# Kernel optimization log

Measured on AMD Instinct MI355X. Metric: run time of the kernel, lower is better.

The kernel has to match this reference:

```python
import jax, jax.numpy as jnp
import numpy as np

ALL_NODE_NUM = 12288
FEA_DIM = 32           # dim2 in DGATNet
BATCH_SIZE = 8
WIN_NUM = 4
POOLED_PER_WIN = 192   # ratio=0.5 of 384 nodes per window graph
N_EDGES = 393216       # avg degree 32


def setup_inputs() -> dict:
    key = jax.random.key(0)
    k1, k2, k3, k4, k5 = jax.random.split(key, 5)
    n_perm = BATCH_SIZE * WIN_NUM * POOLED_PER_WIN  # 6144
    fea = jax.random.normal(k1, (n_perm, FEA_DIM), dtype=jnp.float32)
    # perm: unique sorted node indices kept by the pooling stage
    perm = jnp.sort(jax.random.permutation(k2, ALL_NODE_NUM)[:n_perm]).astype(jnp.int32)
    encoder_edge_index = jax.random.randint(k3, (2, N_EDGES), 0, ALL_NODE_NUM, dtype=jnp.int32)
    encoder_edge_attr = jax.random.uniform(k4, (N_EDGES,), dtype=jnp.float32)
    node_atte_coffe = jax.random.uniform(k5, (BATCH_SIZE * POOLED_PER_WIN,), dtype=jnp.float32)
    return {
        "fea": fea,
        "perm": perm,
        "encoder_edge_index": encoder_edge_index,
        "encoder_edge_attr": encoder_edge_attr,
        "node_atte_coffe": node_atte_coffe,
        "all_node_num": ALL_NODE_NUM,
        "batch_size": BATCH_SIZE,
    }


def reference(fea, perm, encoder_edge_index, encoder_edge_attr, node_atte_coffe,
              all_node_num, batch_size):
    """Faithful JAX translation of DiffusioUnpool.forward (DGATNet.unpool)."""
    n_perm, fea_dim = fea.shape
    slide_win_num = n_perm // node_atte_coffe.shape[0]
    node_num = node_atte_coffe.shape[0] // batch_size

    # ones(B,W,1) @ coffe(B,1,node_num) == tile coefficients over windows
    nac = node_atte_coffe.reshape(batch_size, 1, node_num)
    win_nac = jnp.broadcast_to(nac, (batch_size, slide_win_num, node_num)).reshape(-1)

    # scatter pooled features / coefficients back into the full node set
    x_zero = jnp.zeros((all_node_num, fea_dim), dtype=fea.dtype).at[perm].set(fea)
    atte_zero = jnp.zeros((all_node_num,), dtype=fea.dtype).at[perm].set(win_nac)

    # dense adjacency (duplicate edges sum, as in sparse_coo_tensor + to_dense)
    A = jnp.zeros((all_node_num, all_node_num), dtype=fea.dtype)
    A = A.at[encoder_edge_index[0], encoder_edge_index[1]].add(encoder_edge_attr)
    A = A + jnp.eye(all_node_num, dtype=fea.dtype)  # + I self loops

    d = 1.0 / jnp.sqrt(jnp.sum(A, axis=1))  # diag of D = deg^{-1/2}
    # D A D x  ==  d * (A @ (d * x))
    x = d[:, None] * (A @ (d[:, None] * x_zero))
    atte_updata = d * (A @ (d * atte_zero))
    return x, atte_updata
```

## Files before the change

### kernel.cpp

```cpp
#include <hip/hip_runtime.h>

constexpr int ALL_NODES = 12288;
constexpr int FEA       = 32;
constexpr int N_PERM    = 6144;
constexpr int N_EDGES   = 393216;
constexpr int NODE_NUM  = 192;
constexpr int WINxNODE  = 768;

constexpr int RCAP   = 48;
constexpr int NWORDS = ALL_NODES / 32;
constexpr float FIX   = 16777216.0f;
constexpr float UNFIX = 1.0f / 16777216.0f;

constexpr size_t CNT_OFF    = 0;
constexpr size_t ROWBUF_OFF = CNT_OFF + 2 * (size_t)ALL_NODES;
constexpr size_t BMP_OFF    = ROWBUF_OFF + (size_t)ALL_NODES * RCAP * 2;
constexpr size_t RANK_OFF   = BMP_OFF + NWORDS;

__global__ __launch_bounds__(512) void k_init(const int* __restrict__ perm,
                                              uint4* __restrict__ cnt_v,
                                              unsigned int* __restrict__ bmp,
                                              int* __restrict__ rank) {
    int t = threadIdx.x;
    if (blockIdx.x == 0) {
        __shared__ int pops[NWORDS];
        unsigned bits = 0u;
        if (t < NWORDS) {
            int base = t * 32;
            int loI = 0, hiI = N_PERM;
            while (loI < hiI) {
                int mid = (loI + hiI) >> 1;
                if (perm[mid] < base) loI = mid + 1; else hiI = mid;
            }
            for (int k = loI; k < N_PERM; ++k) {
                int p = perm[k];
                if (p >= base + 32) break;
                bits |= 1u << (p - base);
            }
            bmp[t] = bits;
            pops[t] = __popc(bits);
        }
        __syncthreads();
        for (int off = 1; off < NWORDS; off <<= 1) {
            int v = 0;
            if (t < NWORDS && t >= off) v = pops[t - off];
            __syncthreads();
            if (t < NWORDS) pops[t] += v;
            __syncthreads();
        }
        if (t < NWORDS) rank[t] = pops[t] - __popc(bits);
    } else {
        cnt_v[(blockIdx.x - 1) * 512 + t] = make_uint4(0u, 0u, 0u, 0u);
    }
}

__global__ __launch_bounds__(256) void k_bin(const int* __restrict__ ei0,
                                             const int* __restrict__ ei1,
                                             const float* __restrict__ attr,
                                             const unsigned int* __restrict__ bmp,
                                             const int* __restrict__ rank,
                                             unsigned long long* __restrict__ cnt64,
                                             uint2* __restrict__ rowbuf) {
    int p = blockIdx.x * 256 + threadIdx.x;
    int2   r2 = ((const int2*)ei0)[p];
    int2   c2 = ((const int2*)ei1)[p];
    float2 w2 = ((const float2*)attr)[p];
#pragma unroll
    for (int q = 0; q < 2; ++q) {
        int r = q ? r2.y : r2.x;
        int c = q ? c2.y : c2.x;
        float w = q ? w2.y : w2.x;
        unsigned wfix = __float2uint_rn(w * FIX);
        unsigned word = bmp[c >> 5];
        bool live = (word >> (c & 31)) & 1u;
        unsigned long long add = (unsigned long long)wfix
                               | (live ? (1ULL << 40) : 0ULL);
        unsigned long long old = atomicAdd(cnt64 + r, add);
        if (live) {
            unsigned slot = (unsigned)(old >> 40);
            if (slot < RCAP) {
                int kk = rank[c >> 5] + __popc(word & ((1u << (c & 31)) - 1u));
                rowbuf[(size_t)r * RCAP + slot] =
                    make_uint2(((unsigned)kk << 14) | (unsigned)c, __float_as_uint(w));
            }
        }
    }
}

__device__ __forceinline__ float deg_to_d(unsigned long long cv) {
    unsigned dsum = (unsigned)(cv & 0xFFFFFFFFFFULL);
    return rsqrtf(1.0f + (float)dsum * UNFIX);
}

__global__ __launch_bounds__(256) void k_spmv(const uint2* __restrict__ rowbuf,
                                              const unsigned long long* __restrict__ cnt64,
                                              const float* __restrict__ fea,
                                              const float* __restrict__ nac,
                                              const unsigned int* __restrict__ bmp,
                                              const int* __restrict__ rank,
                                              float* __restrict__ out_x,
                                              float* __restrict__ out_a) {
    int t = threadIdx.x;
    int r = blockIdx.x * 8 + (t >> 5);
    int f = t & 31;
    unsigned long long cv = cnt64[r];
    int n = (int)(cv >> 40); if (n > RCAP) n = RCAP;
    float d_r = deg_to_d(cv);
    const uint2* rp = rowbuf + (size_t)r * RCAP;
    float acc = 0.f, accA = 0.f;
    int i = 0;
    for (; i + 8 <= n; i += 8) {
        uint2 e[8];
#pragma unroll
        for (int q = 0; q < 8; ++q) e[q] = rp[i + q];
        float dci[8], yv[8];
#pragma unroll
        for (int q = 0; q < 8; ++q) {
            dci[q] = deg_to_d(cnt64[e[q].x & 16383]);
            yv[q]  = fea[(size_t)(e[q].x >> 14) * FEA + f];
        }
#pragma unroll
        for (int q = 0; q < 8; ++q)
            acc += __uint_as_float(e[q].y) * dci[q] * yv[q];
        if (f == 0) {
#pragma unroll
            for (int q = 0; q < 8; ++q) {
                int kk = e[q].x >> 14;
                accA += __uint_as_float(e[q].y) * dci[q]
                      * nac[(kk / WINxNODE) * NODE_NUM + (kk % NODE_NUM)];
            }
        }
    }
    for (; i < n; ++i) {
        uint2 e = rp[i];
        int kk = e.x >> 14, c = e.x & 16383;
        float d = deg_to_d(cnt64[c]);
        float w = __uint_as_float(e.y);
        acc += w * d * fea[(size_t)kk * FEA + f];
        if (f == 0)
            accA += w * d * nac[(kk / WINxNODE) * NODE_NUM + (kk % NODE_NUM)];
    }
    unsigned word = bmp[r >> 5];
    float self = 0.f, selfa = 0.f;
    if ((word >> (r & 31)) & 1u) {
        int kkr = rank[r >> 5] + __popc(word & ((1u << (r & 31)) - 1u));
        self  = d_r * fea[(size_t)kkr * FEA + f];
        selfa = d_r * nac[(kkr / WINxNODE) * NODE_NUM + (kkr % NODE_NUM)];
    }
    out_x[(size_t)r * FEA + f] = d_r * (acc + self);
    if (f == 0)
        out_a[r] = d_r * (accA + selfa);
}

extern "C" void kernel_launch(void* const* d_in, const int* in_sizes, int n_in,
                              void* d_out, int out_size, void* d_ws, size_t ws_size,
                              hipStream_t stream) {
    const float* fea  = (const float*)d_in[0];
    const int*   perm = (const int*)d_in[1];
    const int*   ei   = (const int*)d_in[2];
    const float* attr = (const float*)d_in[3];
    const float* nac  = (const float*)d_in[4];

    unsigned int*       ws     = (unsigned int*)d_ws;
    unsigned long long* cnt64  = (unsigned long long*)(ws + CNT_OFF);
    uint2*              rowbuf = (uint2*)(ws + ROWBUF_OFF);
    unsigned int*       bmp    = ws + BMP_OFF;
    int*                rank   = (int*)(ws + RANK_OFF);

    float* out_x = (float*)d_out;
    float* out_a = out_x + ALL_NODES * FEA;

    k_init<<<13,            512, 0, stream>>>(perm, (uint4*)cnt64, bmp, rank);
    k_bin <<<N_EDGES / 512, 256, 0, stream>>>(ei, ei + N_EDGES, attr, bmp, rank,
                                              cnt64, rowbuf);
    k_spmv<<<ALL_NODES / 8, 256, 0, stream>>>(rowbuf, cnt64, fea, nac, bmp, rank,
                                              out_x, out_a);
}
```

Measured before the change: 105.3 us.

## Replicate per-row atomic counters into four copies and precompute degree table

Edge binning now spreads each row's atomic counter and row buffer across four replicas selected by wavefront within the block, which should reduce atomic contention on hot rows. A new kernel sums the replicas into a float degree-normalisation table and packs per-replica edge counts. The SpMV then reads dtab instead of recomputing rsqrt from 64-bit counters, and gathers edges from the four replica segments. This costs an extra launch, a larger workspace to zero, and more index arithmetic in the gather loop. Each replica segment can hold only 24 live edges, so a row whose edges land unevenly across replicas can silently drop entries.

```diff
diff --git a/kernel.cpp b/kernel.cpp
--- a/kernel.cpp
+++ b/kernel.cpp
@@ -7,15 +7,18 @@
 constexpr int NODE_NUM  = 192;
 constexpr int WINxNODE  = 768;
 
-constexpr int RCAP   = 48;
+constexpr int NREP   = 4;
+constexpr int RCAPR  = 24;
 constexpr int NWORDS = ALL_NODES / 32;
 constexpr float FIX   = 16777216.0f;
 constexpr float UNFIX = 1.0f / 16777216.0f;
 
 constexpr size_t CNT_OFF    = 0;
-constexpr size_t ROWBUF_OFF = CNT_OFF + 2 * (size_t)ALL_NODES;
-constexpr size_t BMP_OFF    = ROWBUF_OFF + (size_t)ALL_NODES * RCAP * 2;
+constexpr size_t ROWBUF_OFF = CNT_OFF + 2 * (size_t)NREP * ALL_NODES;
+constexpr size_t BMP_OFF    = ROWBUF_OFF + (size_t)NREP * ALL_NODES * RCAPR * 2;
 constexpr size_t RANK_OFF   = BMP_OFF + NWORDS;
+constexpr size_t DTAB_OFF   = RANK_OFF + NWORDS;
+constexpr size_t NW_OFF     = DTAB_OFF + ALL_NODES;
 
 __global__ __launch_bounds__(512) void k_init(const int* __restrict__ perm,
                                               uint4* __restrict__ cnt_v,
@@ -61,7 +64,9 @@
                                              const int* __restrict__ rank,
                                              unsigned long long* __restrict__ cnt64,
                                              uint2* __restrict__ rowbuf) {
-    int p = blockIdx.x * 256 + threadIdx.x;
+    int t = threadIdx.x;
+    int p = blockIdx.x * 256 + t;
+    int rep = t >> 6;
     int2   r2 = ((const int2*)ei0)[p];
     int2   c2 = ((const int2*)ei1)[p];
     float2 w2 = ((const float2*)attr)[p];
@@ -75,25 +80,39 @@
         bool live = (word >> (c & 31)) & 1u;
         unsigned long long add = (unsigned long long)wfix
                                | (live ? (1ULL << 40) : 0ULL);
-        unsigned long long old = atomicAdd(cnt64 + r, add);
+        size_t rr = (size_t)rep * ALL_NODES + r;
+        unsigned long long old = atomicAdd(cnt64 + rr, add);
         if (live) {
             unsigned slot = (unsigned)(old >> 40);
-            if (slot < RCAP) {
+            if (slot < RCAPR) {
                 int kk = rank[c >> 5] + __popc(word & ((1u << (c & 31)) - 1u));
-                rowbuf[(size_t)r * RCAP + slot] =
+                rowbuf[rr * RCAPR + slot] =
                     make_uint2(((unsigned)kk << 14) | (unsigned)c, __float_as_uint(w));
             }
         }
     }
 }
 
-__device__ __forceinline__ float deg_to_d(unsigned long long cv) {
-    unsigned dsum = (unsigned)(cv & 0xFFFFFFFFFFULL);
-    return rsqrtf(1.0f + (float)dsum * UNFIX);
+__global__ __launch_bounds__(256) void k_deg(const unsigned long long* __restrict__ cnt64,
+                                             float* __restrict__ dtab,
+                                             unsigned int* __restrict__ nwords) {
+    int r = blockIdx.x * 256 + threadIdx.x;
+    unsigned long long c0 = cnt64[r];
+    unsigned long long c1 = cnt64[ALL_NODES + r];
+    unsigned long long c2 = cnt64[2 * ALL_NODES + r];
+    unsigned long long c3 = cnt64[3 * ALL_NODES + r];
+    unsigned long long s = c0 + c1 + c2 + c3;
+    dtab[r] = rsqrtf(1.0f + (float)(unsigned)s * UNFIX);
+    unsigned n0 = (unsigned)(c0 >> 40); if (n0 > RCAPR) n0 = RCAPR;
+    unsigned n1 = (unsigned)(c1 >> 40); if (n1 > RCAPR) n1 = RCAPR;
+    unsigned n2 = (unsigned)(c2 >> 40); if (n2 > RCAPR) n2 = RCAPR;
+    unsigned n3 = (unsigned)(c3 >> 40); if (n3 > RCAPR) n3 = RCAPR;
+    nwords[r] = n0 | (n1 << 8) | (n2 << 16) | (n3 << 24);
 }
 
 __global__ __launch_bounds__(256) void k_spmv(const uint2* __restrict__ rowbuf,
-                                              const unsigned long long* __restrict__ cnt64,
+                                              const float* __restrict__ dtab,
+                                              const unsigned int* __restrict__ nwords,
                                               const float* __restrict__ fea,
                                               const float* __restrict__ nac,
                                               const unsigned int* __restrict__ bmp,
@@ -103,20 +122,27 @@
     int t = threadIdx.x;
     int r = blockIdx.x * 8 + (t >> 5);
     int f = t & 31;
-    unsigned long long cv = cnt64[r];
-    int n = (int)(cv >> 40); if (n > RCAP) n = RCAP;
-    float d_r = deg_to_d(cv);
-    const uint2* rp = rowbuf + (size_t)r * RCAP;
+    float d_r = dtab[r];
+    unsigned nw = nwords[r];
+    int b1 = nw & 255;
+    int b2 = b1 + ((nw >> 8) & 255);
+    int b3 = b2 + ((nw >> 16) & 255);
+    int n  = b3 + (nw >> 24);
     float acc = 0.f, accA = 0.f;
     int i = 0;
     for (; i + 8 <= n; i += 8) {
         uint2 e[8];
 #pragma unroll
-        for (int q = 0; q < 8; ++q) e[q] = rp[i + q];
+        for (int q = 0; q < 8; ++q) {
+            int gi  = i + q;
+            int rep = (gi >= b1) + (gi >= b2) + (gi >= b3);
+            int base = rep == 0 ? 0 : (rep == 1 ? b1 : (rep == 2 ? b2 : b3));
+            e[q] = rowbuf[((size_t)rep * ALL_NODES + r) * RCAPR + (gi - base)];
+        }
         float dci[8], yv[8];
 #pragma unroll
         for (int q = 0; q < 8; ++q) {
-            dci[q] = deg_to_d(cnt64[e[q].x & 16383]);
+            dci[q] = dtab[e[q].x & 16383];
             yv[q]  = fea[(size_t)(e[q].x >> 14) * FEA + f];
         }
 #pragma unroll
@@ -132,9 +158,11 @@
         }
     }
     for (; i < n; ++i) {
-        uint2 e = rp[i];
+        int rep = (i >= b1) + (i >= b2) + (i >= b3);
+        int base = rep == 0 ? 0 : (rep == 1 ? b1 : (rep == 2 ? b2 : b3));
+        uint2 e = rowbuf[((size_t)rep * ALL_NODES + r) * RCAPR + (i - base)];
         int kk = e.x >> 14, c = e.x & 16383;
-        float d = deg_to_d(cnt64[c]);
+        float d = dtab[c];
         float w = __uint_as_float(e.y);
         acc += w * d * fea[(size_t)kk * FEA + f];
         if (f == 0)
@@ -166,13 +194,16 @@
     uint2*              rowbuf = (uint2*)(ws + ROWBUF_OFF);
     unsigned int*       bmp    = ws + BMP_OFF;
     int*                rank   = (int*)(ws + RANK_OFF);
+    float*              dtab   = (float*)(ws + DTAB_OFF);
+    unsigned int*       nwords = ws + NW_OFF;
 
     float* out_x = (float*)d_out;
     float* out_a = out_x + ALL_NODES * FEA;
 
-    k_init<<<13,            512, 0, stream>>>(perm, (uint4*)cnt64, bmp, rank);
+    k_init<<<49,            512, 0, stream>>>(perm, (uint4*)cnt64, bmp, rank);
     k_bin <<<N_EDGES / 512, 256, 0, stream>>>(ei, ei + N_EDGES, attr, bmp, rank,
                                               cnt64, rowbuf);
-    k_spmv<<<ALL_NODES / 8, 256, 0, stream>>>(rowbuf, cnt64, fea, nac, bmp, rank,
+    k_deg <<<ALL_NODES / 256, 256, 0, stream>>>(cnt64, dtab, nwords);
+    k_spmv<<<ALL_NODES / 8, 256, 0, stream>>>(rowbuf, dtab, nwords, fea, nac, bmp, rank,
                                               out_x, out_a);
 }
```

Measured after the change: 111.5 us. 5.9% more time.

## Privatize degree sums in LDS histograms and precompute normalization table

Applied to the files above, without the earlier changes.

Degree sums are no longer built with 64-bit global atomics on every edge. Each block now accumulates a private 12288-entry LDS histogram, writes it to a partials buffer, and a new reduction kernel sums the partials and stores a precomputed deg^-1/2 table. Global atomics are now used only for live-edge slot counters, which are 32-bit. The SpMV reads the float table instead of recomputing rsqrt from 64-bit counters. In exchange there is an extra kernel launch and a roughly 12.5MB partials write and read, and the 48KB LDS histogram per block limits occupancy.

```diff
diff --git a/kernel.cpp b/kernel.cpp
--- a/kernel.cpp
+++ b/kernel.cpp
@@ -9,13 +9,16 @@
 
 constexpr int RCAP   = 48;
 constexpr int NWORDS = ALL_NODES / 32;
+constexpr int NHB    = 256;
 constexpr float FIX   = 16777216.0f;
 constexpr float UNFIX = 1.0f / 16777216.0f;
 
-constexpr size_t CNT_OFF    = 0;
-constexpr size_t ROWBUF_OFF = CNT_OFF + 2 * (size_t)ALL_NODES;
+constexpr size_t CNT32_OFF  = 0;
+constexpr size_t ROWBUF_OFF = CNT32_OFF + (size_t)ALL_NODES;
 constexpr size_t BMP_OFF    = ROWBUF_OFF + (size_t)ALL_NODES * RCAP * 2;
 constexpr size_t RANK_OFF   = BMP_OFF + NWORDS;
+constexpr size_t DTAB_OFF   = RANK_OFF + NWORDS;
+constexpr size_t PART_OFF   = DTAB_OFF + ALL_NODES;
 
 __global__ __launch_bounds__(512) void k_init(const int* __restrict__ perm,
                                               uint4* __restrict__ cnt_v,
@@ -54,30 +57,33 @@
     }
 }
 
-__global__ __launch_bounds__(256) void k_bin(const int* __restrict__ ei0,
+__global__ __launch_bounds__(512) void k_bin(const int* __restrict__ ei0,
                                              const int* __restrict__ ei1,
                                              const float* __restrict__ attr,
                                              const unsigned int* __restrict__ bmp,
                                              const int* __restrict__ rank,
-                                             unsigned long long* __restrict__ cnt64,
-                                             uint2* __restrict__ rowbuf) {
-    int p = blockIdx.x * 256 + threadIdx.x;
-    int2   r2 = ((const int2*)ei0)[p];
-    int2   c2 = ((const int2*)ei1)[p];
-    float2 w2 = ((const float2*)attr)[p];
-#pragma unroll
-    for (int q = 0; q < 2; ++q) {
-        int r = q ? r2.y : r2.x;
-        int c = q ? c2.y : c2.x;
-        float w = q ? w2.y : w2.x;
+                                             unsigned int* __restrict__ cnt32,
+                                             uint2* __restrict__ rowbuf,
+                                             unsigned int* __restrict__ part) {
+    __shared__ unsigned int hist[ALL_NODES];
+    int t = threadIdx.x;
+    uint4* hv = (uint4*)hist;
+#pragma unroll
+    for (int i = 0; i < 6; ++i) hv[t + i * 512] = make_uint4(0u, 0u, 0u, 0u);
+    __syncthreads();
+
+    int base = blockIdx.x * (N_EDGES / NHB);
+#pragma unroll
+    for (int q = 0; q < 3; ++q) {
+        int p = base + q * 512 + t;
+        int   r = ei0[p];
+        int   c = ei1[p];
+        float w = attr[p];
         unsigned wfix = __float2uint_rn(w * FIX);
+        atomicAdd(&hist[r], wfix);
         unsigned word = bmp[c >> 5];
-        bool live = (word >> (c & 31)) & 1u;
-        unsigned long long add = (unsigned long long)wfix
-                               | (live ? (1ULL << 40) : 0ULL);
-        unsigned long long old = atomicAdd(cnt64 + r, add);
-        if (live) {
-            unsigned slot = (unsigned)(old >> 40);
+        if ((word >> (c & 31)) & 1u) {
+            unsigned slot = atomicAdd(cnt32 + r, 1u);
             if (slot < RCAP) {
                 int kk = rank[c >> 5] + __popc(word & ((1u << (c & 31)) - 1u));
                 rowbuf[(size_t)r * RCAP + slot] =
@@ -85,15 +91,33 @@
             }
         }
     }
-}
-
-__device__ __forceinline__ float deg_to_d(unsigned long long cv) {
-    unsigned dsum = (unsigned)(cv & 0xFFFFFFFFFFULL);
-    return rsqrtf(1.0f + (float)dsum * UNFIX);
+    __syncthreads();
+    uint4* pv = (uint4*)(part + (size_t)blockIdx.x * ALL_NODES);
+#pragma unroll
+    for (int i = 0; i < 6; ++i) pv[t + i * 512] = hv[t + i * 512];
+}
+
+__global__ __launch_bounds__(256) void k_deg(const unsigned int* __restrict__ part,
+                                             float* __restrict__ dtab) {
+    __shared__ unsigned int acc[256];
+    int t  = threadIdx.x;
+    int rl = t & 63, s = t >> 6;
+    int r  = blockIdx.x * 64 + rl;
+    unsigned int sum = 0;
+    const unsigned int* p = part + (size_t)(s * 64) * ALL_NODES + r;
+#pragma unroll 8
+    for (int b = 0; b < 64; ++b) sum += p[(size_t)b * ALL_NODES];
+    acc[t] = sum;
+    __syncthreads();
+    if (t < 64) {
+        unsigned int deg = acc[t] + acc[64 + t] + acc[128 + t] + acc[192 + t];
+        dtab[r] = rsqrtf(1.0f + (float)deg * UNFIX);
+    }
 }
 
 __global__ __launch_bounds__(256) void k_spmv(const uint2* __restrict__ rowbuf,
-                                              const unsigned long long* __restrict__ cnt64,
+                                              const unsigned int* __restrict__ cnt32,
+                                              const float* __restrict__ dtab,
                                               const float* __restrict__ fea,
                                               const float* __restrict__ nac,
                                               const unsigned int* __restrict__ bmp,
@@ -103,9 +127,8 @@
     int t = threadIdx.x;
     int r = blockIdx.x * 8 + (t >> 5);
     int f = t & 31;
-    unsigned long long cv = cnt64[r];
-    int n = (int)(cv >> 40); if (n > RCAP) n = RCAP;
-    float d_r = deg_to_d(cv);
+    int n = (int)cnt32[r]; if (n > RCAP) n = RCAP;
+    float d_r = dtab[r];
     const uint2* rp = rowbuf + (size_t)r * RCAP;
     float acc = 0.f, accA = 0.f;
     int i = 0;
@@ -116,7 +139,7 @@
         float dci[8], yv[8];
 #pragma unroll
         for (int q = 0; q < 8; ++q) {
-            dci[q] = deg_to_d(cnt64[e[q].x & 16383]);
+            dci[q] = dtab[e[q].x & 16383];
             yv[q]  = fea[(size_t)(e[q].x >> 14) * FEA + f];
         }
 #pragma unroll
@@ -134,7 +157,7 @@
     for (; i < n; ++i) {
         uint2 e = rp[i];
         int kk = e.x >> 14, c = e.x & 16383;
-        float d = deg_to_d(cnt64[c]);
+        float d = dtab[c];
         float w = __uint_as_float(e.y);
         acc += w * d * fea[(size_t)kk * FEA + f];
         if (f == 0)
@@ -162,17 +185,20 @@
     const float* nac  = (const float*)d_in[4];
 
     unsigned int*       ws     = (unsigned int*)d_ws;
-    unsigned long long* cnt64  = (unsigned long long*)(ws + CNT_OFF);
+    unsigned int*       cnt32  = ws + CNT32_OFF;
     uint2*              rowbuf = (uint2*)(ws + ROWBUF_OFF);
     unsigned int*       bmp    = ws + BMP_OFF;
     int*                rank   = (int*)(ws + RANK_OFF);
+    float*              dtab   = (float*)(ws + DTAB_OFF);
+    unsigned int*       part   = ws + PART_OFF;
 
     float* out_x = (float*)d_out;
     float* out_a = out_x + ALL_NODES * FEA;
 
-    k_init<<<13,            512, 0, stream>>>(perm, (uint4*)cnt64, bmp, rank);
-    k_bin <<<N_EDGES / 512, 256, 0, stream>>>(ei, ei + N_EDGES, attr, bmp, rank,
-                                              cnt64, rowbuf);
-    k_spmv<<<ALL_NODES / 8, 256, 0, stream>>>(rowbuf, cnt64, fea, nac, bmp, rank,
-                                              out_x, out_a);
-}
+    k_init<<<7,               512, 0, stream>>>(perm, (uint4*)cnt32, bmp, rank);
+    k_bin <<<NHB,             512, 0, stream>>>(ei, ei + N_EDGES, attr, bmp, rank,
+                                                cnt32, rowbuf, part);
+    k_deg <<<ALL_NODES / 64,  256, 0, stream>>>(part, dtab);
+    k_spmv<<<ALL_NODES / 8,   256, 0, stream>>>(rowbuf, cnt32, dtab, fea, nac,
+                                                bmp, rank, out_x, out_a);
+}
```

New measurement: 107.8 us. 2.4% more time.

## Fuse init, binning and SpMV into one cooperative kernel with grid syncs

Applied to the files above, without the earlier changes.

Replaces the three separate launches (init bitmap/rank, edge binning with atomics, per-row SpMV) with a single cooperative persistent kernel that uses grid.sync between phases, with the grid sized from occupancy. This is meant to remove launch overhead and inter-kernel gaps. It falls back to the old three-kernel path if the cooperative launch fails. The trade-offs are grid-wide barrier costs, a fixed grid of at most 512 blocks of 512 threads, and unvectorized edge loads in the binning phase.

```diff
diff --git a/kernel.cpp b/kernel.cpp
--- a/kernel.cpp
+++ b/kernel.cpp
@@ -1,4 +1,7 @@
 #include <hip/hip_runtime.h>
+#include <hip/hip_cooperative_groups.h>
+
+namespace cg = cooperative_groups;
 
 constexpr int ALL_NODES = 12288;
 constexpr int FEA       = 32;
@@ -16,6 +19,133 @@
 constexpr size_t ROWBUF_OFF = CNT_OFF + 2 * (size_t)ALL_NODES;
 constexpr size_t BMP_OFF    = ROWBUF_OFF + (size_t)ALL_NODES * RCAP * 2;
 constexpr size_t RANK_OFF   = BMP_OFF + NWORDS;
+
+__device__ __forceinline__ float deg_to_d(unsigned long long cv) {
+    unsigned dsum = (unsigned)(cv & 0xFFFFFFFFFFULL);
+    return rsqrtf(1.0f + (float)dsum * UNFIX);
+}
+
+__global__ __launch_bounds__(512, 4) void k_fused(
+        const float* __restrict__ fea, const int* __restrict__ perm,
+        const int* __restrict__ ei0, const int* __restrict__ ei1,
+        const float* __restrict__ attr, const float* __restrict__ nac,
+        unsigned long long* __restrict__ cnt64, uint2* __restrict__ rowbuf,
+        unsigned int* __restrict__ bmp, int* __restrict__ rank,
+        float* __restrict__ out_x, float* __restrict__ out_a) {
+    cg::grid_group grid = cg::this_grid();
+    const int t     = threadIdx.x;
+    const int b     = blockIdx.x;
+    const int nb    = gridDim.x;
+    const int gtid  = b * 512 + t;
+    const int gsize = nb * 512;
+
+    if (b == 0) {
+        __shared__ int pops[NWORDS];
+        unsigned bits = 0u;
+        if (t < NWORDS) {
+            int base = t * 32;
+            int loI = 0, hiI = N_PERM;
+            while (loI < hiI) {
+                int mid = (loI + hiI) >> 1;
+                if (perm[mid] < base) loI = mid + 1; else hiI = mid;
+            }
+            for (int k = loI; k < N_PERM; ++k) {
+                int p = perm[k];
+                if (p >= base + 32) break;
+                bits |= 1u << (p - base);
+            }
+            bmp[t] = bits;
+            pops[t] = __popc(bits);
+        }
+        __syncthreads();
+        for (int off = 1; off < NWORDS; off <<= 1) {
+            int v = 0;
+            if (t < NWORDS && t >= off) v = pops[t - off];
+            __syncthreads();
+            if (t < NWORDS) pops[t] += v;
+            __syncthreads();
+        }
+        if (t < NWORDS) rank[t] = pops[t] - __popc(bits);
+    } else {
+        int idx = gtid - 512;
+        if (idx < 2 * ALL_NODES / 4)
+            ((uint4*)cnt64)[idx] = make_uint4(0u, 0u, 0u, 0u);
+    }
+    grid.sync();
+
+    for (int e = gtid; e < N_EDGES; e += gsize) {
+        int   r = ei0[e];
+        int   c = ei1[e];
+        float w = attr[e];
+        unsigned wfix = __float2uint_rn(w * FIX);
+        unsigned word = bmp[c >> 5];
+        bool live = (word >> (c & 31)) & 1u;
+        unsigned long long add = (unsigned long long)wfix
+                               | (live ? (1ULL << 40) : 0ULL);
+        unsigned long long old = atomicAdd(cnt64 + r, add);
+        if (live) {
+            unsigned slot = (unsigned)(old >> 40);
+            if (slot < RCAP) {
+                int kk = rank[c >> 5] + __popc(word & ((1u << (c & 31)) - 1u));
+                rowbuf[(size_t)r * RCAP + slot] =
+                    make_uint2(((unsigned)kk << 14) | (unsigned)c, __float_as_uint(w));
+            }
+        }
+    }
+    grid.sync();
+
+    const int f = t & 31;
+    for (int r0 = b * 16; r0 < ALL_NODES; r0 += nb * 16) {
+        int r = r0 + (t >> 5);
+        unsigned long long cv = cnt64[r];
+        int n = (int)(cv >> 40); if (n > RCAP) n = RCAP;
+        float d_r = deg_to_d(cv);
+        const uint2* rp = rowbuf + (size_t)r * RCAP;
+        float acc = 0.f, accA = 0.f;
+        int i = 0;
+        for (; i + 8 <= n; i += 8) {
+            uint2 e[8];
+#pragma unroll
+            for (int q = 0; q < 8; ++q) e[q] = rp[i + q];
+            float dci[8], yv[8];
+#pragma unroll
+            for (int q = 0; q < 8; ++q) {
+                dci[q] = deg_to_d(cnt64[e[q].x & 16383]);
+                yv[q]  = fea[(size_t)(e[q].x >> 14) * FEA + f];
+            }
+#pragma unroll
+            for (int q = 0; q < 8; ++q)
+                acc += __uint_as_float(e[q].y) * dci[q] * yv[q];
+            if (f == 0) {
+#pragma unroll
+                for (int q = 0; q < 8; ++q) {
+                    int kk = e[q].x >> 14;
+                    accA += __uint_as_float(e[q].y) * dci[q]
+                          * nac[(kk / WINxNODE) * NODE_NUM + (kk % NODE_NUM)];
+                }
+            }
+        }
+        for (; i < n; ++i) {
+            uint2 e = rp[i];
+            int kk = e.x >> 14, c = e.x & 16383;
+            float d = deg_to_d(cnt64[c]);
+            float w = __uint_as_float(e.y);
+            acc += w * d * fea[(size_t)kk * FEA + f];
+            if (f == 0)
+                accA += w * d * nac[(kk / WINxNODE) * NODE_NUM + (kk % NODE_NUM)];
+        }
+        unsigned word = bmp[r >> 5];
+        float self = 0.f, selfa = 0.f;
+        if ((word >> (r & 31)) & 1u) {
+            int kkr = rank[r >> 5] + __popc(word & ((1u << (r & 31)) - 1u));
+            self  = d_r * fea[(size_t)kkr * FEA + f];
+            selfa = d_r * nac[(kkr / WINxNODE) * NODE_NUM + (kkr % NODE_NUM)];
+        }
+        out_x[(size_t)r * FEA + f] = d_r * (acc + self);
+        if (f == 0)
+            out_a[r] = d_r * (accA + selfa);
+    }
+}
 
 __global__ __launch_bounds__(512) void k_init(const int* __restrict__ perm,
                                               uint4* __restrict__ cnt_v,
@@ -85,11 +215,6 @@
             }
         }
     }
-}
-
-__device__ __forceinline__ float deg_to_d(unsigned long long cv) {
-    unsigned dsum = (unsigned)(cv & 0xFFFFFFFFFFULL);
-    return rsqrtf(1.0f + (float)dsum * UNFIX);
 }
 
 __global__ __launch_bounds__(256) void k_spmv(const uint2* __restrict__ rowbuf,
@@ -157,7 +282,8 @@
                               hipStream_t stream) {
     const float* fea  = (const float*)d_in[0];
     const int*   perm = (const int*)d_in[1];
-    const int*   ei   = (const int*)d_in[2];
+    const int*   ei0  = (const int*)d_in[2];
+    const int*   ei1  = ei0 + N_EDGES;
     const float* attr = (const float*)d_in[3];
     const float* nac  = (const float*)d_in[4];
 
@@ -170,9 +296,27 @@
     float* out_x = (float*)d_out;
     float* out_a = out_x + ALL_NODES * FEA;
 
-    k_init<<<13,            512, 0, stream>>>(perm, (uint4*)cnt64, bmp, rank);
-    k_bin <<<N_EDGES / 512, 256, 0, stream>>>(ei, ei + N_EDGES, attr, bmp, rank,
-                                              cnt64, rowbuf);
-    k_spmv<<<ALL_NODES / 8, 256, 0, stream>>>(rowbuf, cnt64, fea, nac, bmp, rank,
-                                              out_x, out_a);
-}
+    static int grid_blocks = 0;
+    if (grid_blocks == 0) {
+        int per_cu = 0;
+        if (hipOccupancyMaxActiveBlocksPerMultiprocessor(&per_cu, k_fused, 512, 0)
+                != hipSuccess || per_cu < 1)
+            per_cu = 1;
+        grid_blocks = per_cu * 256;
+        if (grid_blocks > 512) grid_blocks = 512;
+    }
+
+    void* args[] = {(void*)&fea, (void*)&perm, (void*)&ei0, (void*)&ei1,
+                    (void*)&attr, (void*)&nac, (void*)&cnt64, (void*)&rowbuf,
+                    (void*)&bmp, (void*)&rank, (void*)&out_x, (void*)&out_a};
+    hipError_t err = hipLaunchCooperativeKernel((const void*)k_fused,
+                                                dim3(grid_blocks), dim3(512),
+                                                args, 0, stream);
+    if (err != hipSuccess) {
+        k_init<<<13,            512, 0, stream>>>(perm, (uint4*)cnt64, bmp, rank);
+        k_bin <<<N_EDGES / 512, 256, 0, stream>>>(ei0, ei1, attr, bmp, rank,
+                                                  cnt64, rowbuf);
+        k_spmv<<<ALL_NODES / 8, 256, 0, stream>>>(rowbuf, cnt64, fea, nac, bmp,
+                                                  rank, out_x, out_a);
+    }
+}
```

Result: slower. 180.4 us (+71.3%).
